# Kernel optimization log

Measured on AMD Instinct MI355X. Metric: run time of the kernel, lower is better.

## Reference

```python
import jax, jax.numpy as jnp
import numpy as np

B, L = 16, 200
ITEM_N, B_N, C_N = 50000, 100, 500
IH, DB, DC = 96, 16, 16
HID = IH + DB + DC          # 128
NB, NH = 2, 4               # num_blocks, num_heads
DH = HID // NH              # head size 32
TIME_SPAN = 256
NEG = jnp.float32(-2**32 + 1)
EPS = 1e-8


def _ln(x, s, b):
    mu = jnp.mean(x, -1, keepdims=True)
    var = jnp.mean((x - mu) ** 2, -1, keepdims=True)
    return (x - mu) / jnp.sqrt(var + EPS) * s + b


def setup_inputs() -> dict:
    key = jax.random.key(0)
    ks = jax.random.split(key, 40)
    f = lambda k, sh, sc=0.02: jax.random.normal(k, sh, jnp.float32) * sc
    inp = {}
    inp['user_ids'] = jax.random.randint(ks[0], (B,), 0, 1000)
    inp['log_seqs'] = jax.random.randint(ks[1], (B, L), 0, ITEM_N + 1)
    inp['time_matrices'] = jax.random.randint(ks[2], (B, L, L), 0, TIME_SPAN + 1)
    inp['pos_seqs'] = jax.random.randint(ks[3], (B, L), 0, ITEM_N + 1)
    inp['neg_seqs'] = jax.random.randint(ks[4], (B, L), 0, ITEM_N + 1)
    meta_b = jax.random.randint(ks[5], (ITEM_N + 1, 1), 0, B_N + 1)
    meta_c = jax.random.randint(ks[6], (ITEM_N + 1, 1), 0, C_N + 1)
    item_meta = jnp.concatenate([meta_b, meta_c], -1).at[0].set(0)  # row 0 = padding -> (0,0)
    inp['item_meta'] = item_meta
    # embeddings (padding_idx=0 rows zeroed)
    inp['item_emb_W'] = f(ks[7], (ITEM_N + 1, IH)).at[0].set(0.0)
    inp['item_b_W'] = f(ks[8], (B_N + 1, DB)).at[0].set(0.0)
    inp['item_c_W'] = f(ks[9], (C_N + 1, DC)).at[0].set(0.0)
    inp['abs_pos_K_W'] = f(ks[10], (L, HID))
    inp['abs_pos_V_W'] = f(ks[11], (L, HID))
    inp['time_K_W'] = f(ks[12], (TIME_SPAN + 1, HID))
    inp['time_V_W'] = f(ks[13], (TIME_SPAN + 1, HID))
    # per-block params stacked on leading dim NB
    inp['attn_ln_s'] = jnp.ones((NB, HID), jnp.float32)
    inp['attn_ln_b'] = jnp.zeros((NB, HID), jnp.float32)
    inp['Qw'] = f(ks[14], (NB, HID, HID)); inp['Qb'] = f(ks[15], (NB, HID))
    inp['Kw'] = f(ks[16], (NB, HID, HID)); inp['Kb'] = f(ks[17], (NB, HID))
    inp['Vw'] = f(ks[18], (NB, HID, HID)); inp['Vb'] = f(ks[19], (NB, HID))
    inp['fwd_ln_s'] = jnp.ones((NB, HID), jnp.float32)
    inp['fwd_ln_b'] = jnp.zeros((NB, HID), jnp.float32)
    inp['c1w'] = f(ks[20], (NB, HID, HID)); inp['c1b'] = f(ks[21], (NB, HID))
    inp['c2w'] = f(ks[22], (NB, HID, HID)); inp['c2b'] = f(ks[23], (NB, HID))
    inp['last_ln_s'] = jnp.ones((HID,), jnp.float32)
    inp['last_ln_b'] = jnp.zeros((HID,), jnp.float32)
    return inp


def reference(user_ids, log_seqs, time_matrices, pos_seqs, neg_seqs, item_meta,
              item_emb_W, item_b_W, item_c_W, abs_pos_K_W, abs_pos_V_W,
              time_K_W, time_V_W, attn_ln_s, attn_ln_b, Qw, Qb, Kw, Kb, Vw, Vb,
              fwd_ln_s, fwd_ln_b, c1w, c1b, c2w, c2b, last_ln_s, last_ln_b):
    def embed(ids):  # vectorized Item_Meta + concat embedding
        bb = item_meta[ids, 0]
        cc = item_meta[ids, 1]
        return jnp.concatenate([item_emb_W[ids], item_b_W[bb], item_c_W[cc]], -1)

    seqs = embed(log_seqs) * jnp.sqrt(jnp.float32(IH))  # scale by item_emb dim^0.5
    valid = (log_seqs != 0)                              # [B,L]
    seqs = seqs * valid[..., None]

    # abs pos / time-matrix embeddings (dropout = identity at eval)
    posK = abs_pos_K_W.reshape(L, NH, DH).transpose(1, 0, 2)   # [h,L,dh]
    posV = abs_pos_V_W.reshape(L, NH, DH).transpose(1, 0, 2)
    tK = time_K_W[time_matrices].reshape(B, L, L, NH, DH).transpose(0, 3, 1, 2, 4)  # [b,h,i,j,dh]
    tV = time_V_W[time_matrices].reshape(B, L, L, NH, DH).transpose(0, 3, 1, 2, 4)

    causal = jnp.triu(jnp.ones((L, L), bool), k=1)  # True above diagonal -> masked

    def heads(x):  # [B,L,HID] -> [B,h,L,dh]
        return x.reshape(B, L, NH, DH).transpose(0, 2, 1, 3)

    for i in range(NB):
        Qn = _ln(seqs, attn_ln_s[i], attn_ln_b[i])
        q = heads(Qn @ Qw[i] + Qb[i])
        k = heads(seqs @ Kw[i] + Kb[i])
        v = heads(seqs @ Vw[i] + Vb[i])
        aw = (jnp.einsum('bhid,bhjd->bhij', q, k)
              + jnp.einsum('bhid,hjd->bhij', q, posK)
              + jnp.einsum('bhijd,bhid->bhij', tK, q)) / jnp.sqrt(jnp.float32(DH))
        aw = jnp.where(~valid[:, None, :, None], NEG, aw)  # mask padded query rows
        aw = jnp.where(causal[None, None], NEG, aw)        # causal mask
        A = jax.nn.softmax(aw, axis=-1)
        out = (jnp.einsum('bhij,bhjd->bhid', A, v)
               + jnp.einsum('bhij,hjd->bhid', A, posV)
               + jnp.einsum('bhij,bhijd->bhid', A, tV))
        out = out.transpose(0, 2, 1, 3).reshape(B, L, HID)
        seqs = Qn + out
        x = _ln(seqs, fwd_ln_s[i], fwd_ln_b[i])
        seqs = x + (jax.nn.relu(x @ c1w[i] + c1b[i]) @ c2w[i] + c2b[i])
        seqs = seqs * valid[..., None]

    log_feats = _ln(seqs, last_ln_s, last_ln_b)
    pos_logits = jnp.sum(log_feats * embed(pos_seqs), -1)
    neg_logits = jnp.sum(log_feats * embed(neg_seqs), -1)
    return (pos_logits, neg_logits)
```

## Files before the change

### kernel.cpp

```cpp
#include <hip/hip_runtime.h>

#define BB 16
#define LL 200
#define HID 128
#define NH 4
#define DH 32
#define IH 96
#define NROW (BB*LL)
#define LNEPS 1e-8f

__device__ __forceinline__ float embed_val(int id, int col,
                                           const int* __restrict__ meta,
                                           const float* __restrict__ iW,
                                           const float* __restrict__ bW,
                                           const float* __restrict__ cW)
{
    float v;
    if (col < IH)           v = iW[(size_t)id*IH + col];
    else if (col < IH + 16) v = bW[meta[2*id]   *16 + (col-IH)];
    else                    v = cW[meta[2*id+1] *16 + (col-IH-16)];
    return v;
}

__global__ __launch_bounds__(512) void k_emb_lnqkv(
    const int* __restrict__ logs, const int* __restrict__ meta,
    const float* __restrict__ iW, const float* __restrict__ bW,
    const float* __restrict__ cW,
    const float* __restrict__ lns, const float* __restrict__ lnb,
    const float* __restrict__ Qw, const float* __restrict__ Qb,
    const float* __restrict__ Kw, const float* __restrict__ Kb,
    const float* __restrict__ Vw, const float* __restrict__ Vb,
    const float* __restrict__ posK, const float* __restrict__ posV,
    float* __restrict__ Qn, float* __restrict__ qbuf,
    float* __restrict__ kbuf, float* __restrict__ vbuf)
{
    __shared__ float xs[8][HID];
    __shared__ float qn[8][HID];
    __shared__ float red[4][HID];
    int tid = threadIdx.x;
    int g = tid >> 7, col = tid & 127;
    int r0 = blockIdx.x * 8;

    #pragma unroll
    for (int p = 0; p < 2; ++p) {
        int rr = g + p*4;
        int row = r0 + rr;
        int id = logs[row];
        float x = (id == 0) ? 0.f : embed_val(id, col, meta, iW, bW, cW) * 9.797958971132712f;
        xs[rr][col] = x;
        red[g][col] = x;
        __syncthreads();
        for (int off = 64; off; off >>= 1) { if (col < off) red[g][col] += red[g][col+off]; __syncthreads(); }
        float mu = red[g][0] * (1.f/HID);
        __syncthreads();
        float c = x - mu;
        red[g][col] = c*c; __syncthreads();
        for (int off = 64; off; off >>= 1) { if (col < off) red[g][col] += red[g][col+off]; __syncthreads(); }
        float ln = c * rsqrtf(red[g][0]*(1.f/HID) + LNEPS) * lns[col] + lnb[col];
        qn[rr][col] = ln;
        Qn[(size_t)row*HID + col] = ln;
        __syncthreads();
    }

    int rA = 2*g, rB = 2*g + 1;
    float aq0 = Qb[col], aq1 = aq0;
    float ak0 = Kb[col], ak1 = ak0;
    float av0 = Vb[col], av1 = av0;
    const float* q0 = qn[rA]; const float* q1 = qn[rB];
    const float* x0 = xs[rA]; const float* x1 = xs[rB];
    #pragma unroll 8
    for (int kk = 0; kk < HID; ++kk) {
        float wq = Qw[kk*HID + col];
        float wk = Kw[kk*HID + col];
        float wv = Vw[kk*HID + col];
        aq0 += q0[kk]*wq; aq1 += q1[kk]*wq;
        ak0 += x0[kk]*wk; ak1 += x1[kk]*wk;
        av0 += x0[kk]*wv; av1 += x1[kk]*wv;
    }
    int rowA = r0 + rA, rowB = r0 + rB;
    int lA = rowA % LL, lB = rowB % LL;
    qbuf[(size_t)rowA*HID + col] = aq0;
    qbuf[(size_t)rowB*HID + col] = aq1;
    kbuf[(size_t)rowA*HID + col] = ak0 + posK[lA*HID + col];
    kbuf[(size_t)rowB*HID + col] = ak1 + posK[lB*HID + col];
    vbuf[(size_t)rowA*HID + col] = av0 + posV[lA*HID + col];
    vbuf[(size_t)rowB*HID + col] = av1 + posV[lB*HID + col];
}

__global__ __launch_bounds__(1024) void k_attn(
    const float*  __restrict__ q,
    const float4* __restrict__ kp4,
    const float4* __restrict__ vp4,
    const float4* __restrict__ Qn4,
    const float4* __restrict__ tK4,
    const float4* __restrict__ tV4,
    const int* __restrict__ tmat, const int* __restrict__ logs,
    float4* __restrict__ out4)
{
    __shared__ float4 tk_lds[256*8];
    __shared__ float4 tv_lds[256*8];

    int bid = blockIdx.x;
    int h   = bid & 3;
    int i   = 199 - (bid >> 2);
    int tid = threadIdx.x;

    for (int e = tid; e < 2048; e += 1024) {
        int t = e >> 3, s = e & 7;
        int slot = s ^ (t & 7);
        tk_lds[t*8 + slot] = tK4[(size_t)t*32 + h*8 + s];
        tv_lds[t*8 + slot] = tV4[(size_t)t*32 + h*8 + s];
    }
    __syncthreads();

    int b = __builtin_amdgcn_readfirstlane(tid >> 6);
    int lane = tid & 63;
    int row = b*LL + i;
    int valid = (logs[row] != 0);
    int nj = valid ? (i + 1) : LL;

    int g8 = lane & 56;
    int d4 = lane & 7;

    float4 qq = ((const float4*)q)[(size_t)row*32 + h*8 + d4];

    int tsv[4];
    #pragma unroll
    for (int c = 0; c < 4; ++c) {
        int j = c*64 + lane;
        tsv[c] = (j < nj) ? tmat[(size_t)row*LL + j] : 0;
    }

    float ev[4];
    #pragma unroll
    for (int c = 0; c < 4; ++c) {
        float s0 = -INFINITY;
        if (valid) {
            int jbase = c*64 + g8;
            if (jbase < nj) {
                #pragma unroll
                for (int qi = 0; qi < 8; ++qi) {
                    int j = jbase + qi;
                    bool ok = (j < nj);
                    int t = __shfl(tsv[c], g8 + qi);
                    float part = 0.f;
                    if (ok) {
                        float4 kx = kp4[((size_t)(b*LL + j))*32 + h*8 + d4];
                        float4 tx = (t < 256) ? tk_lds[t*8 + (d4 ^ (t & 7))]
                                              : tK4[(size_t)256*32 + h*8 + d4];
                        part = qq.x*(kx.x+tx.x) + qq.y*(kx.y+tx.y)
                             + qq.z*(kx.z+tx.z) + qq.w*(kx.w+tx.w);
                    }
                    part += __shfl_xor(part, 1);
                    part += __shfl_xor(part, 2);
                    part += __shfl_xor(part, 4);
                    if (qi == d4 && ok) s0 = part * 0.17677669529663687f;
                }
            }
        } else {
            if (c*64 + lane < nj) s0 = 0.f;
        }
        ev[c] = s0;
    }

    float m = fmaxf(fmaxf(ev[0], ev[1]), fmaxf(ev[2], ev[3]));
    #pragma unroll
    for (int off = 32; off; off >>= 1) m = fmaxf(m, __shfl_xor(m, off));
    float ssum = 0.f;
    #pragma unroll
    for (int c = 0; c < 4; ++c) {
        int j = c*64 + lane;
        float e = (j < nj) ? __expf(ev[c] - m) : 0.f;
        ev[c] = e; ssum += e;
    }
    #pragma unroll
    for (int off = 32; off; off >>= 1) ssum += __shfl_xor(ssum, off);
    float inv = 1.f / ssum;

    int jc = lane >> 3;
    float4 acc = {0.f, 0.f, 0.f, 0.f};
    #pragma unroll
    for (int c = 0; c < 4; ++c) {
        int jlo = c*64;
        int jhi = (jlo + 64 < nj) ? (jlo + 64) : nj;
        for (int jj = jlo; jj < jhi; jj += 8) {
            int j = jj + jc;
            float a  = __shfl(ev[c],  j & 63);
            int  tsj = __shfl(tsv[c], j & 63);
            if (j < jhi) {
                float4 vx = vp4[((size_t)(b*LL + j))*32 + h*8 + d4];
                float4 tx;
                if (tsj < 256) tx = tv_lds[tsj*8 + (d4 ^ (tsj & 7))];
                else           tx = tV4[(size_t)256*32 + h*8 + d4];
                acc.x += a*(vx.x+tx.x); acc.y += a*(vx.y+tx.y);
                acc.z += a*(vx.z+tx.z); acc.w += a*(vx.w+tx.w);
            }
        }
    }
    #pragma unroll
    for (int off = 8; off < 64; off <<= 1) {
        acc.x += __shfl_xor(acc.x, off);
        acc.y += __shfl_xor(acc.y, off);
        acc.z += __shfl_xor(acc.z, off);
        acc.w += __shfl_xor(acc.w, off);
    }
    if (jc == 0) {
        float4 qn = Qn4[(size_t)row*32 + h*8 + d4];
        float4 o;
        o.x = qn.x + acc.x*inv;
        o.y = qn.y + acc.y*inv;
        o.z = qn.z + acc.z*inv;
        o.w = qn.w + acc.w*inv;
        out4[(size_t)row*32 + h*8 + d4] = o;
    }
}

__global__ __launch_bounds__(512) void k_ffn(
    const float* __restrict__ seqs_in,
    const float* __restrict__ lns, const float* __restrict__ lnb,
    const float* __restrict__ c1w, const float* __restrict__ c1b,
    const float* __restrict__ c2w, const float* __restrict__ c2b,
    const int* __restrict__ logs,
    float* __restrict__ seqs_out)
{
    __shared__ float xs[8][HID];
    __shared__ float h1[8][HID];
    __shared__ float red[4][HID];
    int tid = threadIdx.x;
    int g = tid >> 7, col = tid & 127;
    int r0 = blockIdx.x * 8;

    #pragma unroll
    for (int p = 0; p < 2; ++p) {
        int rr = g + p*4;
        int row = r0 + rr;
        float x = seqs_in[(size_t)row*HID + col];
        red[g][col] = x;
        __syncthreads();
        for (int off = 64; off; off >>= 1) { if (col < off) red[g][col] += red[g][col+off]; __syncthreads(); }
        float mu = red[g][0] * (1.f/HID);
        __syncthreads();
        float c = x - mu;
        red[g][col] = c*c; __syncthreads();
        for (int off = 64; off; off >>= 1) { if (col < off) red[g][col] += red[g][col+off]; __syncthreads(); }
        xs[rr][col] = c * rsqrtf(red[g][0]*(1.f/HID) + LNEPS) * lns[col] + lnb[col];
        __syncthreads();
    }

    int rA = 2*g, rB = 2*g + 1;
    {
        float a0 = c1b[col], a1 = a0;
        const float* x0 = xs[rA]; const float* x1 = xs[rB];
        #pragma unroll 8
        for (int kk = 0; kk < HID; ++kk) {
            float w = c1w[kk*HID + col];
            a0 += x0[kk]*w; a1 += x1[kk]*w;
        }
        h1[rA][col] = fmaxf(a0, 0.f);
        h1[rB][col] = fmaxf(a1, 0.f);
    }
    __syncthreads();

    {
        float a0 = c2b[col], a1 = a0;
        const float* y0 = h1[rA]; const float* y1 = h1[rB];
        #pragma unroll 8
        for (int kk = 0; kk < HID; ++kk) {
            float w = c2w[kk*HID + col];
            a0 += y0[kk]*w; a1 += y1[kk]*w;
        }
        int rowA = r0 + rA, rowB = r0 + rB;
        float o0 = xs[rA][col] + a0;
        float o1 = xs[rB][col] + a1;
        if (logs[rowA] == 0) o0 = 0.f;
        if (logs[rowB] == 0) o1 = 0.f;
        seqs_out[(size_t)rowA*HID + col] = o0;
        seqs_out[(size_t)rowB*HID + col] = o1;
    }
}

__global__ __launch_bounds__(512) void k_lnqkv(
    const float* __restrict__ seqs,
    const float* __restrict__ lns, const float* __restrict__ lnb,
    const float* __restrict__ Qw, const float* __restrict__ Qb,
    const float* __restrict__ Kw, const float* __restrict__ Kb,
    const float* __restrict__ Vw, const float* __restrict__ Vb,
    const float* __restrict__ posK, const float* __restrict__ posV,
    float* __restrict__ Qn, float* __restrict__ qbuf,
    float* __restrict__ kbuf, float* __restrict__ vbuf)
{
    __shared__ float xs[8][HID];
    __shared__ float qn[8][HID];
    __shared__ float red[4][HID];
    int tid = threadIdx.x;
    int g = tid >> 7, col = tid & 127;
    int r0 = blockIdx.x * 8;

    #pragma unroll
    for (int p = 0; p < 2; ++p) {
        int rr = g + p*4;
        int row = r0 + rr;
        float x = seqs[(size_t)row*HID + col];
        xs[rr][col] = x;
        red[g][col] = x;
        __syncthreads();
        for (int off = 64; off; off >>= 1) { if (col < off) red[g][col] += red[g][col+off]; __syncthreads(); }
        float mu = red[g][0] * (1.f/HID);
        __syncthreads();
        float c = x - mu;
        red[g][col] = c*c; __syncthreads();
        for (int off = 64; off; off >>= 1) { if (col < off) red[g][col] += red[g][col+off]; __syncthreads(); }
        float ln = c * rsqrtf(red[g][0]*(1.f/HID) + LNEPS) * lns[col] + lnb[col];
        qn[rr][col] = ln;
        Qn[(size_t)row*HID + col] = ln;
        __syncthreads();
    }

    int rA = 2*g, rB = 2*g + 1;
    float aq0 = Qb[col], aq1 = aq0;
    float ak0 = Kb[col], ak1 = ak0;
    float av0 = Vb[col], av1 = av0;
    const float* q0 = qn[rA]; const float* q1 = qn[rB];
    const float* x0 = xs[rA]; const float* x1 = xs[rB];
    #pragma unroll 8
    for (int kk = 0; kk < HID; ++kk) {
        float wq = Qw[kk*HID + col];
        float wk = Kw[kk*HID + col];
        float wv = Vw[kk*HID + col];
        aq0 += q0[kk]*wq; aq1 += q1[kk]*wq;
        ak0 += x0[kk]*wk; ak1 += x1[kk]*wk;
        av0 += x0[kk]*wv; av1 += x1[kk]*wv;
    }
    int rowA = r0 + rA, rowB = r0 + rB;
    int lA = rowA % LL, lB = rowB % LL;
    qbuf[(size_t)rowA*HID + col] = aq0;
    qbuf[(size_t)rowB*HID + col] = aq1;
    kbuf[(size_t)rowA*HID + col] = ak0 + posK[lA*HID + col];
    kbuf[(size_t)rowB*HID + col] = ak1 + posK[lB*HID + col];
    vbuf[(size_t)rowA*HID + col] = av0 + posV[lA*HID + col];
    vbuf[(size_t)rowB*HID + col] = av1 + posV[lB*HID + col];
}

__global__ __launch_bounds__(512) void k_ffn_logits(
    const float* __restrict__ seqs_in,
    const float* __restrict__ flns, const float* __restrict__ flnb,
    const float* __restrict__ c1w, const float* __restrict__ c1b,
    const float* __restrict__ c2w, const float* __restrict__ c2b,
    const int* __restrict__ logs,
    const float* __restrict__ lls, const float* __restrict__ llb,
    const int* __restrict__ pos, const int* __restrict__ neg,
    const int* __restrict__ meta,
    const float* __restrict__ iW, const float* __restrict__ bW,
    const float* __restrict__ cW,
    float* __restrict__ out)
{
    __shared__ float xs[8][HID];
    __shared__ float h1[8][HID];
    __shared__ float red[4][HID];
    __shared__ float sx[8][HID];
    int tid = threadIdx.x;
    int g = tid >> 7, col = tid & 127;
    int r0 = blockIdx.x * 8;

    #pragma unroll
    for (int p = 0; p < 2; ++p) {
        int rr = g + p*4;
        int row = r0 + rr;
        float x = seqs_in[(size_t)row*HID + col];
        red[g][col] = x;
        __syncthreads();
        for (int off = 64; off; off >>= 1) { if (col < off) red[g][col] += red[g][col+off]; __syncthreads(); }
        float mu = red[g][0] * (1.f/HID);
        __syncthreads();
        float c = x - mu;
        red[g][col] = c*c; __syncthreads();
        for (int off = 64; off; off >>= 1) { if (col < off) red[g][col] += red[g][col+off]; __syncthreads(); }
        xs[rr][col] = c * rsqrtf(red[g][0]*(1.f/HID) + LNEPS) * flns[col] + flnb[col];
        __syncthreads();
    }

    int rA = 2*g, rB = 2*g + 1;
    {
        float a0 = c1b[col], a1 = a0;
        const float* x0 = xs[rA]; const float* x1 = xs[rB];
        #pragma unroll 8
        for (int kk = 0; kk < HID; ++kk) {
            float w = c1w[kk*HID + col];
            a0 += x0[kk]*w; a1 += x1[kk]*w;
        }
        h1[rA][col] = fmaxf(a0, 0.f);
        h1[rB][col] = fmaxf(a1, 0.f);
    }
    __syncthreads();
    {
        float a0 = c2b[col], a1 = a0;
        const float* y0 = h1[rA]; const float* y1 = h1[rB];
        #pragma unroll 8
        for (int kk = 0; kk < HID; ++kk) {
            float w = c2w[kk*HID + col];
            a0 += y0[kk]*w; a1 += y1[kk]*w;
        }
        int rowA = r0 + rA, rowB = r0 + rB;
        float o0 = xs[rA][col] + a0;
        float o1 = xs[rB][col] + a1;
        if (logs[rowA] == 0) o0 = 0.f;
        if (logs[rowB] == 0) o1 = 0.f;
        sx[rA][col] = o0;
        sx[rB][col] = o1;
    }
    __syncthreads();

    #pragma unroll
    for (int p = 0; p < 2; ++p) {
        int rr = g + p*4;
        int row = r0 + rr;
        float x = sx[rr][col];
        red[g][col] = x;
        __syncthreads();
        for (int off = 64; off; off >>= 1) { if (col < off) red[g][col] += red[g][col+off]; __syncthreads(); }
        float mu = red[g][0] * (1.f/HID);
        __syncthreads();
        float c = x - mu;
        red[g][col] = c*c; __syncthreads();
        for (int off = 64; off; off >>= 1) { if (col < off) red[g][col] += red[g][col+off]; __syncthreads(); }
        float f = c * rsqrtf(red[g][0]*(1.f/HID) + LNEPS) * lls[col] + llb[col];
        __syncthreads();

        int pid = pos[row];
        float e = embed_val(pid, col, meta, iW, bW, cW);
        red[g][col] = f * e; __syncthreads();
        for (int off = 64; off; off >>= 1) { if (col < off) red[g][col] += red[g][col+off]; __syncthreads(); }
        if (col == 0) out[row] = red[g][0];
        __syncthreads();

        int nid = neg[row];
        e = embed_val(nid, col, meta, iW, bW, cW);
        red[g][col] = f * e; __syncthreads();
        for (int off = 64; off; off >>= 1) { if (col < off) red[g][col] += red[g][col+off]; __syncthreads(); }
        if (col == 0) out[NROW + row] = red[g][0];
        __syncthreads();
    }
}

extern "C" void kernel_launch(void* const* d_in, const int* in_sizes, int n_in,
                              void* d_out, int out_size, void* d_ws, size_t ws_size,
                              hipStream_t stream)
{
    const int*  logs = (const int*)d_in[1];
    const int*  tmat = (const int*)d_in[2];
    const int*  pos  = (const int*)d_in[3];
    const int*  neg  = (const int*)d_in[4];
    const int*  meta = (const int*)d_in[5];
    const float* iW   = (const float*)d_in[6];
    const float* bW   = (const float*)d_in[7];
    const float* cW   = (const float*)d_in[8];
    const float* posK = (const float*)d_in[9];
    const float* posV = (const float*)d_in[10];
    const float* tK   = (const float*)d_in[11];
    const float* tV   = (const float*)d_in[12];
    const float* attn_s = (const float*)d_in[13];
    const float* attn_b = (const float*)d_in[14];
    const float* Qw = (const float*)d_in[15];
    const float* Qb = (const float*)d_in[16];
    const float* Kw = (const float*)d_in[17];
    const float* Kb = (const float*)d_in[18];
    const float* Vw = (const float*)d_in[19];
    const float* Vb = (const float*)d_in[20];
    const float* fwd_s = (const float*)d_in[21];
    const float* fwd_b = (const float*)d_in[22];
    const float* c1w = (const float*)d_in[23];
    const float* c1b = (const float*)d_in[24];
    const float* c2w = (const float*)d_in[25];
    const float* c2b = (const float*)d_in[26];
    const float* lls = (const float*)d_in[27];
    const float* llb = (const float*)d_in[28];

    const size_t RC = (size_t)NROW * HID;
    float* seqs = (float*)d_ws;
    float* Qn   = seqs + RC;
    float* qbuf = Qn   + RC;
    float* kbuf = qbuf + RC;
    float* vbuf = kbuf + RC;

    const size_t W = (size_t)HID * HID;

    k_emb_lnqkv<<<NROW/8, 512, 0, stream>>>(logs, meta, iW, bW, cW,
                                            attn_s, attn_b,
                                            Qw, Qb, Kw, Kb, Vw, Vb,
                                            posK, posV, Qn, qbuf, kbuf, vbuf);
    k_attn<<<NH*LL, 1024, 0, stream>>>(qbuf, (const float4*)kbuf,
                                       (const float4*)vbuf, (const float4*)Qn,
                                       (const float4*)tK, (const float4*)tV,
                                       tmat, logs, (float4*)seqs);
    k_ffn<<<NROW/8, 512, 0, stream>>>(seqs, fwd_s, fwd_b,
                                      c1w, c1b, c2w, c2b, logs, seqs);
    k_lnqkv<<<NROW/8, 512, 0, stream>>>(seqs, attn_s + HID, attn_b + HID,
                                        Qw + W, Qb + HID, Kw + W, Kb + HID,
                                        Vw + W, Vb + HID,
                                        posK, posV, Qn, qbuf, kbuf, vbuf);
    k_attn<<<NH*LL, 1024, 0, stream>>>(qbuf, (const float4*)kbuf,
                                       (const float4*)vbuf, (const float4*)Qn,
                                       (const float4*)tK, (const float4*)tV,
                                       tmat, logs, (float4*)seqs);
    k_ffn_logits<<<NROW/8, 512, 0, stream>>>(seqs, fwd_s + HID, fwd_b + HID,
                                             c1w + W, c1b + HID, c2w + W, c2b + HID,
                                             logs, lls, llb, pos, neg, meta,
                                             iW, bW, cW, (float*)d_out);
}
```

Measured before the change: 158.5 us.

## Store time embeddings as bf16 in LDS and split attention blocks by batch half

A new pre-pass kernel truncates the time K/V embedding tables to bf16 in workspace. The attention kernel now stages these bf16 tables in LDS (halving shared memory per block) and widens them back to float when reading. Each attention block now covers 8 batches with 512 threads instead of 16 batches with 1024, doubling the grid. The aim is higher occupancy and cheaper LDS staging, at the cost of truncation error in the time embeddings (truncation, not rounding) and one extra kernel launch.

```diff
diff --git a/kernel.cpp b/kernel.cpp
--- a/kernel.cpp
+++ b/kernel.cpp
@@ -20,6 +20,19 @@
     else if (col < IH + 16) v = bW[meta[2*id]   *16 + (col-IH)];
     else                    v = cW[meta[2*id+1] *16 + (col-IH-16)];
     return v;
+}
+
+__device__ __forceinline__ float bf2f(unsigned short u) {
+    return __uint_as_float(((unsigned)u) << 16);
+}
+
+__global__ void k_cvt(const float* __restrict__ tK, const float* __restrict__ tV,
+                      unsigned short* __restrict__ tkb, unsigned short* __restrict__ tvb)
+{
+    int t = blockIdx.x, d = threadIdx.x;
+    size_t idx = (size_t)t*HID + d;
+    tkb[idx] = (unsigned short)(__float_as_uint(tK[idx]) >> 16);
+    tvb[idx] = (unsigned short)(__float_as_uint(tV[idx]) >> 16);
 }
 
 __global__ __launch_bounds__(512) void k_emb_lnqkv(
@@ -87,33 +100,36 @@
     vbuf[(size_t)rowB*HID + col] = av1 + posV[lB*HID + col];
 }
 
-__global__ __launch_bounds__(1024) void k_attn(
+__global__ __launch_bounds__(512) void k_attn(
     const float*  __restrict__ q,
     const float4* __restrict__ kp4,
     const float4* __restrict__ vp4,
     const float4* __restrict__ Qn4,
     const float4* __restrict__ tK4,
     const float4* __restrict__ tV4,
+    const ushort4* __restrict__ tkb4,
+    const ushort4* __restrict__ tvb4,
     const int* __restrict__ tmat, const int* __restrict__ logs,
     float4* __restrict__ out4)
 {
-    __shared__ float4 tk_lds[256*8];
-    __shared__ float4 tv_lds[256*8];
+    __shared__ ushort4 tk_lds[256*8];
+    __shared__ ushort4 tv_lds[256*8];
 
     int bid = blockIdx.x;
     int h   = bid & 3;
-    int i   = 199 - (bid >> 2);
+    int bh  = (bid >> 2) & 1;
+    int i   = 199 - (bid >> 3);
     int tid = threadIdx.x;
 
-    for (int e = tid; e < 2048; e += 1024) {
+    for (int e = tid; e < 2048; e += 512) {
         int t = e >> 3, s = e & 7;
         int slot = s ^ (t & 7);
-        tk_lds[t*8 + slot] = tK4[(size_t)t*32 + h*8 + s];
-        tv_lds[t*8 + slot] = tV4[(size_t)t*32 + h*8 + s];
+        tk_lds[t*8 + slot] = tkb4[(size_t)t*32 + h*8 + s];
+        tv_lds[t*8 + slot] = tvb4[(size_t)t*32 + h*8 + s];
     }
     __syncthreads();
 
-    int b = __builtin_amdgcn_readfirstlane(tid >> 6);
+    int b = __builtin_amdgcn_readfirstlane(tid >> 6) + bh*8;
     int lane = tid & 63;
     int row = b*LL + i;
     int valid = (logs[row] != 0);
@@ -146,10 +162,17 @@
                     float part = 0.f;
                     if (ok) {
                         float4 kx = kp4[((size_t)(b*LL + j))*32 + h*8 + d4];
-                        float4 tx = (t < 256) ? tk_lds[t*8 + (d4 ^ (t & 7))]
-                                              : tK4[(size_t)256*32 + h*8 + d4];
-                        part = qq.x*(kx.x+tx.x) + qq.y*(kx.y+tx.y)
-                             + qq.z*(kx.z+tx.z) + qq.w*(kx.w+tx.w);
+                        float tx0, tx1, tx2, tx3;
+                        if (t < 256) {
+                            ushort4 r = tk_lds[t*8 + (d4 ^ (t & 7))];
+                            tx0 = bf2f(r.x); tx1 = bf2f(r.y);
+                            tx2 = bf2f(r.z); tx3 = bf2f(r.w);
+                        } else {
+                            float4 tf = tK4[(size_t)256*32 + h*8 + d4];
+                            tx0 = tf.x; tx1 = tf.y; tx2 = tf.z; tx3 = tf.w;
+                        }
+                        part = qq.x*(kx.x+tx0) + qq.y*(kx.y+tx1)
+                             + qq.z*(kx.z+tx2) + qq.w*(kx.w+tx3);
                     }
                     part += __shfl_xor(part, 1);
                     part += __shfl_xor(part, 2);
@@ -189,11 +212,17 @@
             int  tsj = __shfl(tsv[c], j & 63);
             if (j < jhi) {
                 float4 vx = vp4[((size_t)(b*LL + j))*32 + h*8 + d4];
-                float4 tx;
-                if (tsj < 256) tx = tv_lds[tsj*8 + (d4 ^ (tsj & 7))];
-                else           tx = tV4[(size_t)256*32 + h*8 + d4];
-                acc.x += a*(vx.x+tx.x); acc.y += a*(vx.y+tx.y);
-                acc.z += a*(vx.z+tx.z); acc.w += a*(vx.w+tx.w);
+                float tx0, tx1, tx2, tx3;
+                if (tsj < 256) {
+                    ushort4 r = tv_lds[tsj*8 + (d4 ^ (tsj & 7))];
+                    tx0 = bf2f(r.x); tx1 = bf2f(r.y);
+                    tx2 = bf2f(r.z); tx3 = bf2f(r.w);
+                } else {
+                    float4 tf = tV4[(size_t)256*32 + h*8 + d4];
+                    tx0 = tf.x; tx1 = tf.y; tx2 = tf.z; tx3 = tf.w;
+                }
+                acc.x += a*(vx.x+tx0); acc.y += a*(vx.y+tx1);
+                acc.z += a*(vx.z+tx2); acc.w += a*(vx.w+tx3);
             }
         }
     }
@@ -481,27 +510,33 @@
     float* qbuf = Qn   + RC;
     float* kbuf = qbuf + RC;
     float* vbuf = kbuf + RC;
+    unsigned short* tkb = (unsigned short*)(vbuf + RC);
+    unsigned short* tvb = tkb + 257*HID;
 
     const size_t W = (size_t)HID * HID;
+
+    k_cvt<<<257, 128, 0, stream>>>(tK, tV, tkb, tvb);
 
     k_emb_lnqkv<<<NROW/8, 512, 0, stream>>>(logs, meta, iW, bW, cW,
                                             attn_s, attn_b,
                                             Qw, Qb, Kw, Kb, Vw, Vb,
                                             posK, posV, Qn, qbuf, kbuf, vbuf);
-    k_attn<<<NH*LL, 1024, 0, stream>>>(qbuf, (const float4*)kbuf,
-                                       (const float4*)vbuf, (const float4*)Qn,
-                                       (const float4*)tK, (const float4*)tV,
-                                       tmat, logs, (float4*)seqs);
+    k_attn<<<NH*LL*2, 512, 0, stream>>>(qbuf, (const float4*)kbuf,
+                                        (const float4*)vbuf, (const float4*)Qn,
+                                        (const float4*)tK, (const float4*)tV,
+                                        (const ushort4*)tkb, (const ushort4*)tvb,
+                                        tmat, logs, (float4*)seqs);
     k_ffn<<<NROW/8, 512, 0, stream>>>(seqs, fwd_s, fwd_b,
                                       c1w, c1b, c2w, c2b, logs, seqs);
     k_lnqkv<<<NROW/8, 512, 0, stream>>>(seqs, attn_s + HID, attn_b + HID,
                                         Qw + W, Qb + HID, Kw + W, Kb + HID,
                                         Vw + W, Vb + HID,
                                         posK, posV, Qn, qbuf, kbuf, vbuf);
-    k_attn<<<NH*LL, 1024, 0, stream>>>(qbuf, (const float4*)kbuf,
-                                       (const float4*)vbuf, (const float4*)Qn,
-                                       (const float4*)tK, (const float4*)tV,
-                                       tmat, logs, (float4*)seqs);
+    k_attn<<<NH*LL*2, 512, 0, stream>>>(qbuf, (const float4*)kbuf,
+                                        (const float4*)vbuf, (const float4*)Qn,
+                                        (const float4*)tK, (const float4*)tV,
+                                        (const ushort4*)tkb, (const ushort4*)tvb,
+                                        tmat, logs, (float4*)seqs);
     k_ffn_logits<<<NROW/8, 512, 0, stream>>>(seqs, fwd_s + HID, fwd_b + HID,
                                              c1w + W, c1b + HID, c2w + W, c2b + HID,
                                              logs, lls, llb, pos, neg, meta,
```

Result: faster. 146.3 us (-7.7%).
